# Performance work log

Measured on AMD Instinct MI355X. Metric: run time of the kernel, lower is better.

The kernel has to match this reference:

```python
import jax, jax.numpy as jnp
import numpy as np

N_R, N_U, N_P = 40000, 30000, 30000
N = N_R + N_U + N_P
E = 1600000
NFEAT, NHID, NCLASS = 128, 128, 40


def setup_inputs() -> dict:
    key = jax.random.key(0)
    ks = jax.random.split(key, 12)
    s = 0.05
    return {
        "inputx_r": jax.random.normal(ks[0], (N_R, 5), jnp.float32),
        "inputx_u": jax.random.normal(ks[1], (N_U, 7), jnp.float32),
        "inputx_p": jax.random.normal(ks[2], (N_P, 6), jnp.float32),
        "edge_index": jax.random.randint(ks[3], (2, E), 0, N, jnp.int64)
            if jax.config.jax_enable_x64 else jax.random.randint(ks[3], (2, E), 0, N, jnp.int32),
        "W_r": jax.random.normal(ks[4], (5, NFEAT), jnp.float32) * s,
        "b_r": jax.random.normal(ks[5], (NFEAT,), jnp.float32) * s,
        "W_u": jax.random.normal(ks[6], (7, NFEAT), jnp.float32) * s,
        "b_u": jax.random.normal(ks[7], (NFEAT,), jnp.float32) * s,
        "W_p": jax.random.normal(ks[8], (6, NFEAT), jnp.float32) * s,
        "b_p": jax.random.normal(ks[9], (NFEAT,), jnp.float32) * s,
        "W1": jax.random.normal(ks[10], (NFEAT, NHID), jnp.float32) * s,
        "W2": jax.random.normal(ks[11], (NHID, NCLASS), jnp.float32) * s,
    }


def _gcn_conv(x, W, src, dst, num_nodes):
    # GCNConv(add_self_loops=False, normalize=False, bias=False):
    # out = A @ (x @ W), unit edge weights, aggregation at dst of source messages.
    h = x @ W                                      # [N, d_out]
    return jax.ops.segment_sum(h[src], dst, num_segments=num_nodes)


def reference(inputx_r, inputx_u, inputx_p, edge_index,
              W_r, b_r, W_u, b_u, W_p, b_p, W1, W2):
    # Segment-wise input projections (nums = [[N_R, N_R+N_U], [.,.], [.,.]]
    # with empty 2nd/3rd blocks; tail is the p-segment), then two GCN layers.
    x = jnp.concatenate([
        inputx_r @ W_r + b_r,   # nodes [0 : N_R]
        inputx_u @ W_u + b_u,   # nodes [N_R : N_R+N_U]
        inputx_p @ W_p + b_p,   # nodes [N_R+N_U : N]
    ], axis=0)                  # [N, NFEAT]
    src, dst = edge_index[0], edge_index[1]
    h = jax.nn.relu(_gcn_conv(x, W1, src, dst, N))   # gc1 + relu
    # dropout: inference (training=False) -> identity
    out = _gcn_conv(h, W2, src, dst, N)              # gc2
    return out
```

## Files before the change

kernel.cpp:

```cpp
#include <hip/hip_runtime.h>

constexpr int kNR = 40000;
constexpr int kNU = 30000;
constexpr int kNP = 30000;
constexpr int kN  = 100000;
constexpr int kE  = 1600000;
constexpr int kF  = 128;
constexpr int kC  = 40;
constexpr int kBN = 64;
constexpr int kNB = (kN + kBN - 1) / kBN;
constexpr int kNBp = 1600;
constexpr int kSlot = 2048;
constexpr int kPackB = 98;
constexpr int kFuseB = kPackB;
constexpr int kW2B   = kPackB + 1;
constexpr int kScat0 = kPackB + 2;
constexpr int kScatB = 256;
constexpr int kCE    = kE / kScatB;
constexpr int kEPT   = (kCE + 1023) / 1024;
constexpr int kPrepB = kScat0 + kScatB;
constexpr int kPl  = 8;
constexpr int kPC  = 5;
constexpr int kNPB = 256;
constexpr int kGBn = (kN + kNPB - 1) / kNPB;
constexpr int kGB  = kPl * kGBn;

typedef __attribute__((ext_vector_type(8))) short bf16x8;
typedef __attribute__((ext_vector_type(4))) float f32x4;

__device__ __forceinline__ float bf_to_f(unsigned short h) {
    union { unsigned int i; float f; } u; u.i = ((unsigned int)h) << 16; return u.f;
}
__device__ __forceinline__ unsigned short f_to_bf(float f) {
    union { unsigned int i; float f; } u; u.f = f;
    unsigned int r = u.i + 0x7FFFu + ((u.i >> 16) & 1u);
    return (unsigned short)(r >> 16);
}
__device__ __forceinline__ float2 bf2_to_f2(unsigned int p) {
    union { unsigned int i; float f; } lo, hi;
    lo.i = (p & 0xFFFFu) << 16;
    hi.i = p & 0xFFFF0000u;
    return make_float2(lo.f, hi.f);
}
__device__ __forceinline__ unsigned int pack_bf2(float a, float b) {
    return (unsigned int)f_to_bf(a) | ((unsigned int)f_to_bf(b) << 16);
}
__device__ __forceinline__ float ldf(const void* p, int i, int isbf) {
    return isbf ? bf_to_f(((const unsigned short*)p)[i]) : ((const float*)p)[i];
}
__device__ __forceinline__ int lde(const int* p, int i, int is64) {
    return is64 ? p[2 * i] : p[i];
}

__device__ __forceinline__ int sniff_isbf(const void* W1, int t, int* sh) {
    if (t < 64) {
        unsigned int wv = ((const unsigned int*)W1)[t];
        unsigned int ax = wv & 0x7FFFu;
        int pl = (ax == 0u) || (ax > 0x2000u && ax < 0x4000u);
        unsigned long long mk = __ballot(pl);
        if (t == 0) *sh = (__popcll(mk) >= 48) ? 1 : 0;
    }
    __syncthreads();
    return *sh;
}

__global__ void __launch_bounds__(1024) gcn_prep(
        const void* __restrict__ xr, const void* __restrict__ xu, const void* __restrict__ xp,
        const void* __restrict__ Wr, const void* __restrict__ br,
        const void* __restrict__ Wu, const void* __restrict__ bu,
        const void* __restrict__ Wp, const void* __restrict__ bp,
        const void* __restrict__ W1, const void* __restrict__ W2,
        const int* __restrict__ ei,
        unsigned short* __restrict__ fwfrag, unsigned short* __restrict__ w2frag,
        uint4* __restrict__ xpack, int* __restrict__ gcnt,
        unsigned int* __restrict__ slots) {
    __shared__ __align__(16) char smem[29696];
    __shared__ int sflag;
    int t = threadIdx.x;
    int bx = blockIdx.x;
    if (bx < kPackB) {
        int isbf = sniff_isbf(W1, t, &sflag);
        int n = bx * 1024 + t;
        if (n >= kN) return;
        const void* base; int roff, d;
        if (n < kNR)            { base = xr; roff = n * 5;               d = 5; }
        else if (n < kNR + kNU) { base = xu; roff = (n - kNR) * 7;       d = 7; }
        else                    { base = xp; roff = (n - kNR - kNU) * 6; d = 6; }
        float f[8];
        #pragma unroll
        for (int i = 0; i < 8; i++) f[i] = (i < d) ? ldf(base, roff + i, isbf) : 0.f;
        uint4 u;
        u.x = pack_bf2(f[0], f[1]);  u.y = pack_bf2(f[2], f[3]);
        u.z = pack_bf2(f[4], f[5]);  u.w = pack_bf2(f[6], f[7]);
        xpack[n] = u;
    } else if (bx == kFuseB) {
        int isbf = sniff_isbf(W1, t, &sflag);
        float* sw   = (float*)smem;
        float* pacc = (float*)(smem + 10752);
        unsigned short* flds = (unsigned short*)(smem + 21504);
        for (int i = t; i < 21 * kF; i += 1024) {
            int r = i >> 7, c = i & 127;
            float v;
            if (r < 5)        v = ldf(Wr, r * kF + c, isbf);
            else if (r < 12)  v = ldf(Wu, (r - 5) * kF + c, isbf);
            else if (r < 18)  v = ldf(Wp, (r - 12) * kF + c, isbf);
            else if (r == 18) v = ldf(br, c, isbf);
            else if (r == 19) v = ldf(bu, c, isbf);
            else              v = ldf(bp, c, isbf);
            sw[i] = v;
        }
        __syncthreads();
        {
            bool active = (t < 256);
            int j = t & 127, half = (t >> 7) & 1;
            float acc[21];
            #pragma unroll
            for (int r = 0; r < 21; r++) acc[r] = 0.f;
            if (active) {
                int k0 = half * 64, k1 = k0 + 64;
                for (int k = k0; k < k1; k++) {
                    float w1 = ldf(W1, k * kF + j, isbf);
                    #pragma unroll
                    for (int r = 0; r < 21; r++) acc[r] += sw[r * kF + k] * w1;
                }
            }
            if (active && half == 1) {
                #pragma unroll
                for (int r = 0; r < 21; r++) pacc[r * kF + j] = acc[r];
            }
            __syncthreads();
            if (active && half == 0) {
                #pragma unroll
                for (int r = 0; r < 21; r++) acc[r] += pacc[r * kF + j];
                unsigned short row[32];
                #pragma unroll
                for (int s = 0; s < 32; s++) row[s] = 0;
                #pragma unroll
                for (int i = 0; i < 5; i++) row[0  + i] = f_to_bf(acc[i]);
                #pragma unroll
                for (int i = 0; i < 7; i++) row[8  + i] = f_to_bf(acc[5 + i]);
                #pragma unroll
                for (int i = 0; i < 6; i++) row[16 + i] = f_to_bf(acc[12 + i]);
                row[24] = f_to_bf(acc[18]);  row[25] = f_to_bf(acc[19]);  row[26] = f_to_bf(acc[20]);
                #pragma unroll
                for (int s = 0; s < 32; s++) flds[j * 32 + s] = row[s];
            }
        }
        __syncthreads();
        for (int idx = t; idx < 8 * 64; idx += 1024) {
            int t8 = idx >> 6, lane = idx & 63;
            int mm = lane & 15, q = lane >> 4;
            #pragma unroll
            for (int j = 0; j < 8; j++)
                fwfrag[idx * 8 + j] = flds[(16 * t8 + mm) * 32 + q * 8 + j];
        }
    } else if (bx == kW2B) {
        int isbf = sniff_isbf(W1, t, &sflag);
        for (int idx = t; idx < 12 * 64; idx += 1024) {
            int st = idx >> 6, lane = idx & 63;
            int s = st / 3, tt = st % 3;
            int mm = lane & 15, q = lane >> 4;
            int cls = 16 * tt + mm;
            #pragma unroll
            for (int j = 0; j < 8; j++) {
                int k = s * 32 + q * 8 + j;
                w2frag[idx * 8 + j] = (cls < kC) ? f_to_bf(ldf(W2, k * kC + cls, isbf))
                                                 : (unsigned short)0;
            }
        }
    } else {
        int* hist = (int*)smem;
        int* cur  = (int*)(smem + 6400);
        if (t < 64) {
            int v = ((const int*)ei)[2 * t + 1];
            unsigned long long mk = __ballot(v != 0);
            if (t == 0) sflag = (mk == 0ull) ? 1 : 0;
        }
        for (int i = t; i < kNBp; i += 1024) hist[i] = 0;
        __syncthreads();
        int is64 = sflag;
        int blk = bx - kScat0;
        int e0 = blk * kCE, e1 = e0 + kCE;
        unsigned int dv[kEPT], sv[kEPT];
        #pragma unroll
        for (int it = 0; it < kEPT; it++) {
            int e = e0 + t + it * 1024;
            bool ok = (e < e1);
            dv[it] = ok ? (unsigned int)lde(ei, kE + e, is64) : 0xFFFFFFFFu;
            sv[it] = ok ? (unsigned int)lde(ei, e, is64) : 0u;
        }
        #pragma unroll
        for (int it = 0; it < kEPT; it++)
            if (dv[it] < (unsigned int)kN) atomicAdd(&hist[dv[it] >> 6], 1);
        __syncthreads();
        int off = (blk * 401) % kNBp;
        for (int j = t; j < kNBp; j += 1024) {
            int i = j + off;
            if (i >= kNBp) i -= kNBp;
            int h = hist[i];
            cur[i] = (h > 0) ? atomicAdd(&gcnt[i], h) : 0;
        }
        __syncthreads();
        #pragma unroll
        for (int it = 0; it < kEPT; it++) {
            if (dv[it] < (unsigned int)kN) {
                unsigned int sval = (sv[it] < (unsigned int)kN) ? sv[it] : 0u;
                int b = (int)(dv[it] >> 6);
                int pos = atomicAdd(&cur[b], 1);
                if (pos < kSlot) slots[(size_t)b * kSlot + pos] = (sval << 6) | (dv[it] & 63u);
            }
        }
    }
}

__global__ void __launch_bounds__(256) GCN_2190433321521_kernel(
        const unsigned int* __restrict__ slots,
        const int* __restrict__ gcnt,
        const uint4* __restrict__ xpack,
        const unsigned short* __restrict__ fwfrag,
        const unsigned short* __restrict__ w2frag,
        int* __restrict__ rpb,
        int* __restrict__ rpe,
        int* __restrict__ col,
        uint4* __restrict__ hpl) {
    __shared__ __align__(16) char smem[25600];
    float*          agg_l  = (float*)smem;
    int*            cnt_l  = (int*)(smem + 7424);
    int*            strt_l = (int*)(smem + 7680);
    int*            cntv_l = (int*)(smem + 7936);
    unsigned int*   wst    = (unsigned int*)(smem + 8192);
    int*            col_l  = (int*)(smem + 16384);
    unsigned short* hbuf   = (unsigned short*)(smem + 8192);
    unsigned short* cst    = (unsigned short*)smem;

    int b = blockIdx.x;
    int base = b * kBN;
    int nn = min(kBN, kN - base);
    int tid = threadIdx.x;

    if (tid < kBN) cnt_l[tid] = 0;
    __syncthreads();
    int p0 = b * kSlot;
    int m = min(gcnt[b], kSlot);
    int p1 = p0 + m;

    for (int ib = p0 + tid; ib < p1; ib += 1024) {
        unsigned int w[4]; int ok[4];
        #pragma unroll
        for (int j = 0; j < 4; j++) {
            int i = ib + j * 256;
            ok[j] = (i < p1);
            w[j] = ok[j] ? slots[i] : 0u;
        }
        #pragma unroll
        for (int j = 0; j < 4; j++) {
            int i = ib + j * 256;
            if (ok[j]) {
                wst[i - p0] = w[j];
                atomicAdd(&cnt_l[w[j] & 63u], 1);
            }
        }
    }
    __syncthreads();
    if (tid < 64) {
        int v = cnt_l[tid];
        int incl = v;
        #pragma unroll
        for (int o = 1; o < 64; o <<= 1) {
            int y = __shfl_up(incl, o, 64);
            if (tid >= o) incl += y;
        }
        int cursor = p0 + incl - v;
        cnt_l[tid]  = cursor;
        strt_l[tid] = cursor;
        cntv_l[tid] = v;
        if (tid < nn) { rpb[base + tid] = cursor; rpe[base + tid] = cursor + v; }
    }
    __syncthreads();

    for (int i = p0 + tid; i < p1; i += 256) {
        unsigned int w = wst[i - p0];
        unsigned int s = w >> 6;
        int dloc = (int)(w & 63u);
        int pos = atomicAdd(&cnt_l[dloc], 1);
        col_l[pos - p0] = (int)s;
    }
    __syncthreads();
    for (int i = tid; i < m; i += 256) col[p0 + i] = col_l[i];

    {
        int node = tid >> 2, j = tid & 3;
        float aR[8], aU[8], aP[8];
        #pragma unroll
        for (int i = 0; i < 8; i++) { aR[i] = 0.f; aU[i] = 0.f; aP[i] = 0.f; }
        float cR = 0.f, cU = 0.f, cP = 0.f;
        int start = strt_l[node] - p0;
        int c = cntv_l[node];
        for (int i = start + j; i < start + c; i += 4) {
            int s = col_l[i];
            uint4 u = xpack[s];
            float2 q0 = bf2_to_f2(u.x), q1 = bf2_to_f2(u.y);
            float2 q2 = bf2_to_f2(u.z), q3 = bf2_to_f2(u.w);
            if (s < kNR) {
                aR[0]+=q0.x; aR[1]+=q0.y; aR[2]+=q1.x; aR[3]+=q1.y;
                aR[4]+=q2.x; aR[5]+=q2.y; aR[6]+=q3.x; aR[7]+=q3.y; cR += 1.f;
            } else if (s < kNR + kNU) {
                aU[0]+=q0.x; aU[1]+=q0.y; aU[2]+=q1.x; aU[3]+=q1.y;
                aU[4]+=q2.x; aU[5]+=q2.y; aU[6]+=q3.x; aU[7]+=q3.y; cU += 1.f;
            } else {
                aP[0]+=q0.x; aP[1]+=q0.y; aP[2]+=q1.x; aP[3]+=q1.y;
                aP[4]+=q2.x; aP[5]+=q2.y; aP[6]+=q3.x; aP[7]+=q3.y; cP += 1.f;
            }
        }
        #pragma unroll
        for (int i2 = 0; i2 < 8; i2++) {
            float v = aR[i2];
            v += __shfl_xor(v, 1, 64);  v += __shfl_xor(v, 2, 64);
            if (j == 0) agg_l[node * 29 + i2] = v;
        }
        #pragma unroll
        for (int i2 = 0; i2 < 8; i2++) {
            float v = aU[i2];
            v += __shfl_xor(v, 1, 64);  v += __shfl_xor(v, 2, 64);
            if (j == 0) agg_l[node * 29 + 8 + i2] = v;
        }
        #pragma unroll
        for (int i2 = 0; i2 < 8; i2++) {
            float v = aP[i2];
            v += __shfl_xor(v, 1, 64);  v += __shfl_xor(v, 2, 64);
            if (j == 0) agg_l[node * 29 + 16 + i2] = v;
        }
        float v = cR;
        v += __shfl_xor(v, 1, 64);  v += __shfl_xor(v, 2, 64);
        if (j == 0) agg_l[node * 29 + 24] = v;
        v = cU;
        v += __shfl_xor(v, 1, 64);  v += __shfl_xor(v, 2, 64);
        if (j == 0) agg_l[node * 29 + 25] = v;
        v = cP;
        v += __shfl_xor(v, 1, 64);  v += __shfl_xor(v, 2, 64);
        if (j == 0) agg_l[node * 29 + 26] = v;
    }
    __syncthreads();

    int wid = tid >> 6, lane = tid & 63;
    int mm = lane & 15, q = lane >> 4;
    int node = wid * 16 + mm;
    bf16x8 a1;
    #pragma unroll
    for (int j = 0; j < 8; j++) {
        int sl = q * 8 + j;
        a1[j] = (sl < 27) ? (short)f_to_bf(agg_l[node * 29 + sl]) : (short)0;
    }
    __syncthreads();
    const bf16x8* fwf = (const bf16x8*)fwfrag;
    f32x4 c1[8];
    #pragma unroll
    for (int t = 0; t < 8; t++) {
        f32x4 z = {0.f, 0.f, 0.f, 0.f};
        c1[t] = __builtin_amdgcn_mfma_f32_16x16x32_bf16(a1, fwf[t * 64 + lane], z, 0, 0, 0);
    }
    unsigned short* hb = hbuf + wid * 16 * 136;
    #pragma unroll
    for (int t = 0; t < 8; t++) {
        #pragma unroll
        for (int r = 0; r < 4; r++)
            hb[(q * 4 + r) * 136 + 16 * t + mm] = f_to_bf(fmaxf(c1[t][r], 0.f));
    }
    const bf16x8* w2f = (const bf16x8*)w2frag;
    f32x4 c2[3];
    #pragma unroll
    for (int t = 0; t < 3; t++) { c2[t].x = 0.f; c2[t].y = 0.f; c2[t].z = 0.f; c2[t].w = 0.f; }
    #pragma unroll
    for (int s = 0; s < 4; s++) {
        bf16x8 a2 = *(const bf16x8*)&hb[mm * 136 + s * 32 + q * 8];
        #pragma unroll
        for (int t = 0; t < 3; t++)
            c2[t] = __builtin_amdgcn_mfma_f32_16x16x32_bf16(a2, w2f[(s * 3 + t) * 64 + lane],
                                                            c2[t], 0, 0, 0);
    }
    #pragma unroll
    for (int t = 0; t < 3; t++) {
        int cls = 16 * t + mm;
        if (cls < kC) {
            #pragma unroll
            for (int r = 0; r < 4; r++)
                cst[(wid * 16 + q * 4 + r) * kC + cls] = f_to_bf(c2[t][r]);
        }
    }
    __syncthreads();
    for (int idx = tid; idx < kPl * kBN; idx += 256) {
        int p = idx >> 6, i = idx & 63;
        if (i < nn) {
            const unsigned short* cr = &cst[i * kC + p * kPC];
            uint4 v;
            v.x = (unsigned)cr[0] | ((unsigned)cr[1] << 16);
            v.y = (unsigned)cr[2] | ((unsigned)cr[3] << 16);
            v.z = (unsigned)cr[4];
            v.w = 0u;
            hpl[(size_t)p * kN + base + i] = v;
        }
    }
}

__global__ void __launch_bounds__(256) gcn_gather2(const uint4* __restrict__ hpl,
                                                   const int* __restrict__ rpb,
                                                   const int* __restrict__ rpe,
                                                   const int* __restrict__ col,
                                                   void* __restrict__ out,
                                                   const void* __restrict__ W1) {
    __shared__ int sisbf;
    int t = threadIdx.x;
    int isbf = sniff_isbf(W1, t, &sisbf);
    int plane = blockIdx.x & 7;
    int nb0 = (blockIdx.x >> 3) * kNPB;
    const uint4* hp = hpl + (size_t)plane * kN;
    int j = t & 3;
    #pragma unroll
    for (int pass = 0; pass < kNPB / 64; pass++) {
        int n = nb0 + pass * 64 + (t >> 2);
        if (n < kN) {
            int beg = rpb[n], end = rpe[n];
            float a0 = 0.f, a1 = 0.f, a2 = 0.f, a3 = 0.f, a4 = 0.f;
            for (int e = beg + j; e < end; e += 4) {
                int s = col[e];
                uint4 u = hp[s];
                float2 q0 = bf2_to_f2(u.x), q1 = bf2_to_f2(u.y);
                a0 += q0.x; a1 += q0.y; a2 += q1.x; a3 += q1.y;
                a4 += bf_to_f((unsigned short)(u.z & 0xFFFFu));
            }
            a0 += __shfl_xor(a0, 1, 64);  a0 += __shfl_xor(a0, 2, 64);
            a1 += __shfl_xor(a1, 1, 64);  a1 += __shfl_xor(a1, 2, 64);
            a2 += __shfl_xor(a2, 1, 64);  a2 += __shfl_xor(a2, 2, 64);
            a3 += __shfl_xor(a3, 1, 64);  a3 += __shfl_xor(a3, 2, 64);
            a4 += __shfl_xor(a4, 1, 64);  a4 += __shfl_xor(a4, 2, 64);
            if (j == 0) {
                if (isbf) {
                    unsigned short* ob = (unsigned short*)out + (size_t)n * kC + plane * kPC;
                    ob[0] = f_to_bf(a0);  ob[1] = f_to_bf(a1);  ob[2] = f_to_bf(a2);
                    ob[3] = f_to_bf(a3);  ob[4] = f_to_bf(a4);
                } else {
                    float* of = (float*)out + (size_t)n * kC + plane * kPC;
                    of[0] = a0;  of[1] = a1;  of[2] = a2;  of[3] = a3;  of[4] = a4;
                }
            }
        }
    }
}

extern "C" void kernel_launch(void* const* d_in, const int* in_sizes, int n_in,
                              void* d_out, int out_size, void* d_ws, size_t ws_size,
                              hipStream_t stream) {
    const void* xr = d_in[0];
    const void* xu = d_in[1];
    const void* xp = d_in[2];
    const int*  ei = (const int*)d_in[3];
    const void* Wr = d_in[4];
    const void* br = d_in[5];
    const void* Wu = d_in[6];
    const void* bu = d_in[7];
    const void* Wp = d_in[8];
    const void* bp = d_in[9];
    const void* W1 = d_in[10];
    const void* W2 = d_in[11];
    (void)in_sizes; (void)n_in; (void)out_size; (void)ws_size;

    char* ws = (char*)d_ws;
    size_t off = 0;
    auto alloc = [&](size_t bytes) -> void* {
        void* p = (void*)(ws + off);
        off = (off + bytes + 255) & ~(size_t)255;
        return p;
    };
    int*            gcnt   = (int*)           alloc((size_t)kNBp * 4);
    unsigned short* fwfrag = (unsigned short*)alloc(8 * 64 * 8 * 2);
    unsigned short* w2frag = (unsigned short*)alloc(12 * 64 * 8 * 2);
    uint4*          xpack  = (uint4*)         alloc((size_t)kN * 16);
    unsigned int*   slots  = (unsigned int*)  alloc((size_t)kNB * kSlot * 4);
    int*            col    = (int*)           alloc((size_t)kNB * kSlot * 4);
    int*            rpb    = (int*)           alloc((size_t)kN * 4);
    int*            rpe    = (int*)           alloc((size_t)kN * 4);
    uint4*          hpl    = (uint4*)         alloc((size_t)kPl * kN * 16);

    hipMemsetAsync(gcnt, 0, (size_t)kNBp * 4, stream);
    gcn_prep<<<kPrepB, 1024, 0, stream>>>(xr, xu, xp, Wr, br, Wu, bu, Wp, bp, W1, W2,
                                          ei, fwfrag, w2frag, xpack, gcnt, slots);
    GCN_2190433321521_kernel<<<kNB, 256, 0, stream>>>(slots, gcnt, xpack, fwfrag, w2frag,
                                                      rpb, rpe, col, hpl);
    gcn_gather2<<<kGB, 256, 0, stream>>>(hpl, rpb, rpe, col, d_out, W1);
}
```

Measured before the change: 214.4 us.

## Repack layer-2 features into 4 dense planes and gather one node per wavefront

The layer-2 message buffer changes from 8 planes of padded 16-byte records (5 bf16 classes each) to 4 planes of dense 20-byte records (10 bf16 classes each). The second gather now gives each wavefront one destination node, with 12 edge lanes times 5 word lanes and shuffle reductions. Its fp32 partials go to a scratch buffer, and a new merge kernel converts them and writes the final output. The goal is to cut padding waste and the number of gather passes over the edge list, at the cost of an extra kernel launch and a scratch round trip. Assigning one node per wave may also underuse lanes on low-degree nodes.

```diff
diff --git a/kernel.cpp b/kernel.cpp
--- a/kernel.cpp
+++ b/kernel.cpp
@@ -19,11 +19,10 @@
 constexpr int kCE    = kE / kScatB;
 constexpr int kEPT   = (kCE + 1023) / 1024;
 constexpr int kPrepB = kScat0 + kScatB;
-constexpr int kPl  = 8;
-constexpr int kPC  = 5;
-constexpr int kNPB = 256;
-constexpr int kGBn = (kN + kNPB - 1) / kNPB;
-constexpr int kGB  = kPl * kGBn;
+constexpr int kPl  = 4;
+constexpr int kPC  = 10;
+constexpr int kGK  = 12500;
+constexpr int kGatB = 8 * kGK;
 
 typedef __attribute__((ext_vector_type(8))) short bf16x8;
 typedef __attribute__((ext_vector_type(4))) float f32x4;
@@ -222,7 +221,7 @@
         int* __restrict__ rpb,
         int* __restrict__ rpe,
         int* __restrict__ col,
-        uint4* __restrict__ hpl) {
+        unsigned int* __restrict__ hpl) {
     __shared__ __align__(16) char smem[25600];
     float*          agg_l  = (float*)smem;
     int*            cnt_l  = (int*)(smem + 7424);
@@ -388,61 +387,83 @@
         }
     }
     __syncthreads();
-    for (int idx = tid; idx < kPl * kBN; idx += 256) {
-        int p = idx >> 6, i = idx & 63;
-        if (i < nn) {
-            const unsigned short* cr = &cst[i * kC + p * kPC];
-            uint4 v;
-            v.x = (unsigned)cr[0] | ((unsigned)cr[1] << 16);
-            v.y = (unsigned)cr[2] | ((unsigned)cr[3] << 16);
-            v.z = (unsigned)cr[4];
-            v.w = 0u;
-            hpl[(size_t)p * kN + base + i] = v;
-        }
-    }
-}
-
-__global__ void __launch_bounds__(256) gcn_gather2(const uint4* __restrict__ hpl,
+    {
+        const unsigned int* cs32 = (const unsigned int*)cst;
+        #pragma unroll
+        for (int p = 0; p < kPl; p++) {
+            for (int i = tid; i < nn * 5; i += 256) {
+                int row = i / 5, cp = i % 5;
+                hpl[(size_t)p * kN * 5 + (size_t)(base + row) * 5 + cp]
+                    = cs32[row * 20 + p * 5 + cp];
+            }
+        }
+    }
+}
+
+__global__ void __launch_bounds__(256) gcn_gather2(const unsigned int* __restrict__ hpl,
                                                    const int* __restrict__ rpb,
                                                    const int* __restrict__ rpe,
                                                    const int* __restrict__ col,
-                                                   void* __restrict__ out,
-                                                   const void* __restrict__ W1) {
+                                                   float* __restrict__ op) {
+    int bid = blockIdx.x;
+    int r = bid & 7;
+    int plane = r & 3;
+    int half = r >> 2;
+    int k = bid >> 3;
+    int t = threadIdx.x;
+    int wid = t >> 6, lane = t & 63;
+    int n = (half * kGK + k) * 4 + wid;
+    const unsigned int* hp = hpl + (size_t)plane * kN * 5;
+    int grp = lane / 5;
+    int cp  = lane % 5;
+    int beg = rpb[n], end = rpe[n];
+    float f0 = 0.f, f1 = 0.f;
+    if (grp < 12) {
+        int e = beg + grp;
+        int c0 = (e      < end) ? col[e]      : -1;
+        int c1 = (e + 12 < end) ? col[e + 12] : -1;
+        if (c0 >= 0) { float2 a = bf2_to_f2(hp[(size_t)c0 * 5 + cp]); f0 += a.x; f1 += a.y; }
+        if (c1 >= 0) { float2 a = bf2_to_f2(hp[(size_t)c1 * 5 + cp]); f0 += a.x; f1 += a.y; }
+        for (e += 24; e < end; e += 12) {
+            float2 a = bf2_to_f2(hp[(size_t)col[e] * 5 + cp]);
+            f0 += a.x; f1 += a.y;
+        }
+    }
+    f0 += __shfl(f0, lane + 30, 64);  f1 += __shfl(f1, lane + 30, 64);
+    f0 += __shfl(f0, lane + 15, 64);  f1 += __shfl(f1, lane + 15, 64);
+    f0 += __shfl(f0, lane + 5, 64) + __shfl(f0, lane + 10, 64);
+    f1 += __shfl(f1, lane + 5, 64) + __shfl(f1, lane + 10, 64);
+    if (lane < 5) {
+        float* o = op + ((size_t)plane * kN + n) * kPC;
+        o[2 * cp]     = f0;
+        o[2 * cp + 1] = f1;
+    }
+}
+
+__global__ void __launch_bounds__(256) gcn_merge(const float* __restrict__ op,
+                                                 unsigned int* __restrict__ out,
+                                                 const void* __restrict__ W1) {
     __shared__ int sisbf;
     int t = threadIdx.x;
     int isbf = sniff_isbf(W1, t, &sisbf);
-    int plane = blockIdx.x & 7;
-    int nb0 = (blockIdx.x >> 3) * kNPB;
-    const uint4* hp = hpl + (size_t)plane * kN;
-    int j = t & 3;
-    #pragma unroll
-    for (int pass = 0; pass < kNPB / 64; pass++) {
-        int n = nb0 + pass * 64 + (t >> 2);
-        if (n < kN) {
-            int beg = rpb[n], end = rpe[n];
-            float a0 = 0.f, a1 = 0.f, a2 = 0.f, a3 = 0.f, a4 = 0.f;
-            for (int e = beg + j; e < end; e += 4) {
-                int s = col[e];
-                uint4 u = hp[s];
-                float2 q0 = bf2_to_f2(u.x), q1 = bf2_to_f2(u.y);
-                a0 += q0.x; a1 += q0.y; a2 += q1.x; a3 += q1.y;
-                a4 += bf_to_f((unsigned short)(u.z & 0xFFFFu));
-            }
-            a0 += __shfl_xor(a0, 1, 64);  a0 += __shfl_xor(a0, 2, 64);
-            a1 += __shfl_xor(a1, 1, 64);  a1 += __shfl_xor(a1, 2, 64);
-            a2 += __shfl_xor(a2, 1, 64);  a2 += __shfl_xor(a2, 2, 64);
-            a3 += __shfl_xor(a3, 1, 64);  a3 += __shfl_xor(a3, 2, 64);
-            a4 += __shfl_xor(a4, 1, 64);  a4 += __shfl_xor(a4, 2, 64);
-            if (j == 0) {
-                if (isbf) {
-                    unsigned short* ob = (unsigned short*)out + (size_t)n * kC + plane * kPC;
-                    ob[0] = f_to_bf(a0);  ob[1] = f_to_bf(a1);  ob[2] = f_to_bf(a2);
-                    ob[3] = f_to_bf(a3);  ob[4] = f_to_bf(a4);
-                } else {
-                    float* of = (float*)out + (size_t)n * kC + plane * kPC;
-                    of[0] = a0;  of[1] = a1;  of[2] = a2;  of[3] = a3;  of[4] = a4;
-                }
-            }
+    int n = blockIdx.x * 256 + t;
+    if (n >= kN) return;
+    if (isbf) {
+        #pragma unroll
+        for (int p = 0; p < kPl; p++) {
+            const float* src = op + ((size_t)p * kN + n) * kPC;
+            #pragma unroll
+            for (int c = 0; c < 5; c++)
+                out[n * 20 + p * 5 + c] = pack_bf2(src[2 * c], src[2 * c + 1]);
+        }
+    } else {
+        float* of = (float*)out;
+        #pragma unroll
+        for (int p = 0; p < kPl; p++) {
+            const float* src = op + ((size_t)p * kN + n) * kPC;
+            #pragma unroll
+            for (int c = 0; c < kPC; c++)
+                of[n * kC + p * kPC + c] = src[c];
         }
     }
 }
@@ -479,12 +500,14 @@
     int*            col    = (int*)           alloc((size_t)kNB * kSlot * 4);
     int*            rpb    = (int*)           alloc((size_t)kN * 4);
     int*            rpe    = (int*)           alloc((size_t)kN * 4);
-    uint4*          hpl    = (uint4*)         alloc((size_t)kPl * kN * 16);
+    unsigned int*   hpl    = (unsigned int*)  alloc((size_t)kPl * kN * 5 * 4);
+    float*          op     = (float*)         alloc((size_t)kPl * kN * kPC * 4);
 
     hipMemsetAsync(gcnt, 0, (size_t)kNBp * 4, stream);
     gcn_prep<<<kPrepB, 1024, 0, stream>>>(xr, xu, xp, Wr, br, Wu, bu, Wp, bp, W1, W2,
                                           ei, fwfrag, w2frag, xpack, gcnt, slots);
     GCN_2190433321521_kernel<<<kNB, 256, 0, stream>>>(slots, gcnt, xpack, fwfrag, w2frag,
                                                       rpb, rpe, col, hpl);
-    gcn_gather2<<<kGB, 256, 0, stream>>>(hpl, rpb, rpe, col, d_out, W1);
-}
+    gcn_gather2<<<kGatB, 256, 0, stream>>>(hpl, rpb, rpe, col, op);
+    gcn_merge<<<(kN + 255) / 256, 256, 0, stream>>>(op, (unsigned int*)d_out, W1);
+}
```

Result: slower. 238.2 us (+11.1%).
